# Optimization experiments

Measured on AMD Instinct MI355X. Metric: run time of the kernel, lower is better.

## Reference

```python
import jax, jax.numpy as jnp
import numpy as np


def _mha(q, k, v, num_heads):
    # q,k,v: [B, L, C] -> multi-head attention, scale = 1/sqrt(head_dim)
    B, Lq, C = q.shape
    Lk = k.shape[1]
    d = C // num_heads
    qh = q.reshape(B, Lq, num_heads, d)
    kh = k.reshape(B, Lk, num_heads, d)
    vh = v.reshape(B, Lk, num_heads, d)
    scale = 1.0 / jnp.sqrt(jnp.asarray(d, q.dtype))
    scores = jnp.einsum('blhd,bmhd->bhlm', qh, kh) * scale
    probs = jax.nn.softmax(scores, axis=-1)
    out = jnp.einsum('bhlm,bmhd->blhd', probs, vh)
    return out.reshape(B, Lq, C)


def setup_inputs() -> dict:
    key = jax.random.key(0)
    ks = jax.random.split(key, 9)
    b, n, f, l, C = 1, 4, 8, 256, 320
    s = 0.02
    return {
        'hidden_states': jax.random.normal(ks[0], (b * n * f, l, C), jnp.float32),
        'Wq': jax.random.normal(ks[1], (C, C), jnp.float32) * s,
        'Wk': jax.random.normal(ks[2], (C, C), jnp.float32) * s,
        'Wv': jax.random.normal(ks[3], (C, C), jnp.float32) * s,
        'Wo': jax.random.normal(ks[4], (C, C), jnp.float32) * s,
        'bo': jnp.zeros((C,), jnp.float32),
        'Wq_i2v': jax.random.normal(ks[5], (C, C), jnp.float32) * s,
        'Wo_i2v': jax.random.normal(ks[6], (C, C), jnp.float32) * s,
        'bo_i2v': jnp.zeros((C,), jnp.float32),
        'num_heads': 8,
        'num_views': 4,
        'num_frames': 8,
    }


def reference(hidden_states, Wq, Wk, Wv, Wo, bo, Wq_i2v, Wo_i2v, bo_i2v,
              num_heads, num_views, num_frames):
    BNF, l, C = hidden_states.shape
    n, f = num_views, num_frames
    b = BNF // (n * f)
    # '(b n f) l c -> (b f) (n l) c'
    h = hidden_states.reshape(b, n, f, l, C).transpose(0, 2, 1, 3, 4).reshape(b * f, n * l, C)
    L = n * l

    q = h @ Wq
    k = h @ Wk
    v = h @ Wv

    # first-frame KV broadcast across all frames within the same b
    k_first = jnp.broadcast_to(k.reshape(b, f, L, C)[:, 0:1], (b, f, L, C)).reshape(b * f, L, C)
    v_first = jnp.broadcast_to(v.reshape(b, f, L, C)[:, 0:1], (b, f, L, C)).reshape(b * f, L, C)

    base = _mha(q, k, v, num_heads)

    q_i2v = h @ Wq_i2v
    i2v = _mha(q_i2v, k_first, v_first, num_heads)
    i2v = i2v @ Wo_i2v + bo_i2v

    out = (base + i2v) @ Wo + bo

    # '(b f) (n l) c -> (b n f) l c'
    out = out.reshape(b, f, n, l, C).transpose(0, 2, 1, 3, 4).reshape(b * n * f, l, C)
    return out
```

## Files before the change

kernel.cpp:

```cpp
#include <hip/hip_runtime.h>
#include <hip/hip_bf16.h>

#define MROWS 8192
#define CDIM  320
#define QPAD  512

typedef __attribute__((ext_vector_type(8))) short bf16x8;
typedef __attribute__((ext_vector_type(4))) float f32x4;

__device__ __forceinline__ unsigned bfbits(float x) {
  union { float f; unsigned u; } a; a.f = x;
  return a.u + 0x8000u;
}
__device__ __forceinline__ void splitbf(float x, short& hi, short& lo) {
  unsigned hu = bfbits(x) & 0xffff0000u;
  union { unsigned u; float f; } h; h.u = hu;
  hi = (short)(hu >> 16);
  lo = (short)(bfbits(x - h.f) >> 16);
}
__device__ __forceinline__ unsigned pk_bf16(float a, float b) {
  union { __hip_bfloat162 h2; unsigned u; } cv;
  cv.h2 = __float22bfloat162_rn(float2{a, b});
  return cv.u;
}

__device__ __forceinline__ void cp16_g2l(const void* g, void* l) {
  __builtin_amdgcn_global_load_lds(
      (const __attribute__((address_space(1))) void*)g,
      (__attribute__((address_space(3))) void*)l, 16, 0, 0);
}

__device__ __forceinline__ int swizzle_row(int r) {
  int ff = r >> 10;
  int t  = r & 1023;
  int nn = t >> 8;
  int ll = t & 255;
  return nn * 2048 + ff * 256 + ll;
}

__global__ __launch_bounds__(256) void wc_kernel(
    const float* __restrict__ Woi, const float* __restrict__ Wo,
    float* __restrict__ Wc)
{
  const int r0 = blockIdx.x * 64, c0 = blockIdx.y * 64;
  __shared__ float As[64][36];
  __shared__ float Bs[32][68];
  const int tid = threadIdx.x, tx = tid & 15, ty = tid >> 4;
  float acc[4][4] = {};

  const int ra = tid >> 3, kq = (tid & 7) * 4;
  const int kb = tid >> 4, cq = (tid & 15) * 4;

  for (int k0 = 0; k0 < 320; k0 += 32) {
    float4 a1 = *(const float4*)(Woi + (size_t)(r0 + ra) * 320 + k0 + kq);
    float4 a2 = *(const float4*)(Woi + (size_t)(r0 + ra + 32) * 320 + k0 + kq);
    float4 b1 = *(const float4*)(Wo + (size_t)(k0 + kb) * 320 + c0 + cq);
    float4 b2 = *(const float4*)(Wo + (size_t)(k0 + kb + 16) * 320 + c0 + cq);
    __syncthreads();
    *(float4*)&As[ra][kq] = a1;
    *(float4*)&As[ra + 32][kq] = a2;
    *(float4*)&Bs[kb][cq] = b1;
    *(float4*)&Bs[kb + 16][cq] = b2;
    __syncthreads();
    #pragma unroll
    for (int kk = 0; kk < 32; ++kk) {
      float4 bv = *(const float4*)&Bs[kk][tx * 4];
      #pragma unroll
      for (int i = 0; i < 4; ++i) {
        float a = As[ty * 4 + i][kk];
        acc[i][0] = fmaf(a, bv.x, acc[i][0]);
        acc[i][1] = fmaf(a, bv.y, acc[i][1]);
        acc[i][2] = fmaf(a, bv.z, acc[i][2]);
        acc[i][3] = fmaf(a, bv.w, acc[i][3]);
      }
    }
  }
  #pragma unroll
  for (int i = 0; i < 4; ++i) {
    float4 v = make_float4(acc[i][0], acc[i][1], acc[i][2], acc[i][3]);
    *(float4*)(Wc + (size_t)(r0 + ty * 4 + i) * 320 + c0 + tx * 4) = v;
  }
}

__global__ __launch_bounds__(256) void pack_kernel(
    const float* __restrict__ hidden,
    const float* __restrict__ Wq, const float* __restrict__ Wk,
    const float* __restrict__ Wv, const float* __restrict__ Wqi,
    const float* __restrict__ Wo, const float* __restrict__ Wc,
    const float* __restrict__ bo, const float* __restrict__ boi,
    short* __restrict__ Ah, short* __restrict__ Al,
    short* __restrict__ WTh, short* __restrict__ WTl,
    short* __restrict__ WFh, short* __restrict__ WFl,
    float* __restrict__ bc,
    short* __restrict__ Qp, short* __restrict__ Kp, short* __restrict__ Qip,
    float qscale)
{
  const int b = blockIdx.x, tid = threadIdx.x;
  if (b < 64) {
    const int r0 = b * 128;
    for (int e = tid; e < 128 * 80; e += 256) {
      int r = e / 80, cq = (e % 80) * 4;
      float4 x = *(const float4*)(hidden + (size_t)swizzle_row(r0 + r) * 320 + cq);
      union { ushort4 v; short s[4]; } h, l;
      splitbf(x.x, h.s[0], l.s[0]); splitbf(x.y, h.s[1], l.s[1]);
      splitbf(x.z, h.s[2], l.s[2]); splitbf(x.w, h.s[3], l.s[3]);
      *(ushort4*)&Ah[(size_t)(r0 + r) * 320 + cq] = h.v;
      *(ushort4*)&Al[(size_t)(r0 + r) * 320 + cq] = l.v;
    }
  } else if (b < 128) {
    const int t2 = b - 64, wi = t2 >> 4, seg = t2 & 15;
    const float* W = wi == 0 ? Wq : wi == 1 ? Wk : wi == 2 ? Wv : Wqi;
    const float s = (wi == 0 || wi == 3) ? qscale : 1.0f;
    short* th = WTh + (size_t)wi * 320 * 320;
    short* tl = WTl + (size_t)wi * 320 * 320;
    for (int e = tid; e < 20 * 320; e += 256) {
      int n = seg * 20 + e / 320, k = e % 320;
      short hi, lo;
      splitbf(W[(size_t)k * 320 + n] * s, hi, lo);
      th[(size_t)n * 320 + k] = hi;
      tl[(size_t)n * 320 + k] = lo;
    }
  } else if (b < 160) {
    const int t2 = b - 128;
    for (int e = tid; e < 10 * 640; e += 256) {
      int n = t2 * 10 + e / 640, k = e % 640;
      float x = (k < 320) ? Wo[(size_t)k * 320 + n] : Wc[(size_t)(k - 320) * 320 + n];
      short hi, lo;
      splitbf(x, hi, lo);
      WFh[(size_t)n * 640 + k] = hi;
      WFl[(size_t)n * 640 + k] = lo;
    }
  } else if (b < 168) {
    const int n = (b - 160) * 40 + tid;
    if (tid < 40) {
      float s = bo[n];
      for (int j = 0; j < 320; ++j) s = fmaf(boi[j], Wo[(size_t)j * 320 + n], s);
      bc[n] = s;
    }
  } else {
    const int bz = b - 168, buf = bz >> 5, seg = bz & 31;
    short* P = buf == 0 ? Qp : buf == 1 ? Kp : Qip;
    const uint4 z = make_uint4(0, 0, 0, 0);
    for (int e = tid; e < 256 * 24; e += 256) {
      int row = (seg << 8) + (e / 24);
      int cc = e % 24, h = cc / 3, c3 = cc % 3;
      *(uint4*)&P[(size_t)row * QPAD + h * 64 + 40 + c3 * 8] = z;
    }
  }
}

__global__ __launch_bounds__(256, 3) void mfma_gemm(
    const short* __restrict__ Ah, const short* __restrict__ Al,
    const short* __restrict__ BTh, const short* __restrict__ BTl,
    int K, int mode,
    short* __restrict__ Qp, short* __restrict__ Kp,
    short* __restrict__ Vt, short* __restrict__ Qip,
    float* __restrict__ Of, const float* __restrict__ bias)
{
  const int tid  = threadIdx.x;
  const int wave = tid >> 6;
  const int lane = tid & 63;
  const int quad = lane >> 4;
  const int l16  = lane & 15;
  const int row0 = blockIdx.x * 128;

  const short *bth, *btl;
  int nbase, wi = 0;
  if (mode == 0) {
    const int ct = blockIdx.y;
    wi = ct / 5;
    bth = BTh + (size_t)wi * 320 * 320;
    btl = BTl + (size_t)wi * 320 * 320;
    nbase = (ct % 5) * 64;
  } else {
    bth = BTh; btl = BTl;
    nbase = blockIdx.y * 64;
  }

  __shared__ short Ash[128][32], Asl[128][32];
  __shared__ short Bsh[64][32],  Bsl[64][32];

  f32x4 acc[2][4];
  #pragma unroll
  for (int mt = 0; mt < 2; ++mt)
    #pragma unroll
    for (int nt = 0; nt < 4; ++nt) acc[mt][nt] = (f32x4){0.f, 0.f, 0.f, 0.f};

  const int lr = lane >> 2, lc = (lane & 3) * 8;
  const short* gah = Ah + (size_t)(row0 + wave * 16 + lr) * K + lc;
  const short* gal = Al ? Al + (size_t)(row0 + wave * 16 + lr) * K + lc : nullptr;
  const short* gbh = bth + (size_t)(nbase + wave * 16 + lr) * K + lc;
  const short* gbl = btl + (size_t)(nbase + wave * 16 + lr) * K + lc;
  short* lah1 = &Ash[wave * 16][0];
  short* lah2 = &Ash[64 + wave * 16][0];
  short* lal1 = &Asl[wave * 16][0];
  short* lal2 = &Asl[64 + wave * 16][0];
  short* lbh  = &Bsh[wave * 16][0];
  short* lbl  = &Bsl[wave * 16][0];

  for (int k0 = 0; k0 < K; k0 += 32) {
    __syncthreads();
    cp16_g2l(gah + k0, lah1);
    cp16_g2l(gah + (size_t)64 * K + k0, lah2);
    if (Al) {
      cp16_g2l(gal + k0, lal1);
      cp16_g2l(gal + (size_t)64 * K + k0, lal2);
    }
    cp16_g2l(gbh + k0, lbh);
    cp16_g2l(gbl + k0, lbl);
    __syncthreads();

    bf16x8 afh[2], afl[2], bfh[4], bfl[4];
    #pragma unroll
    for (int mt = 0; mt < 2; ++mt) {
      afh[mt] = *(const bf16x8*)&Ash[wave * 32 + mt * 16 + l16][quad * 8];
      if (Al) afl[mt] = *(const bf16x8*)&Asl[wave * 32 + mt * 16 + l16][quad * 8];
    }
    #pragma unroll
    for (int nt = 0; nt < 4; ++nt) {
      bfh[nt] = *(const bf16x8*)&Bsh[nt * 16 + l16][quad * 8];
      bfl[nt] = *(const bf16x8*)&Bsl[nt * 16 + l16][quad * 8];
    }
    #pragma unroll
    for (int mt = 0; mt < 2; ++mt)
      #pragma unroll
      for (int nt = 0; nt < 4; ++nt) {
        acc[mt][nt] = __builtin_amdgcn_mfma_f32_16x16x32_bf16(afh[mt], bfh[nt], acc[mt][nt], 0, 0, 0);
        acc[mt][nt] = __builtin_amdgcn_mfma_f32_16x16x32_bf16(afh[mt], bfl[nt], acc[mt][nt], 0, 0, 0);
        if (Al)
          acc[mt][nt] = __builtin_amdgcn_mfma_f32_16x16x32_bf16(afl[mt], bfh[nt], acc[mt][nt], 0, 0, 0);
      }
  }

  if (mode == 0) {
    if (wi == 2) {
      #pragma unroll
      for (int mt = 0; mt < 2; ++mt)
        #pragma unroll
        for (int nt = 0; nt < 4; ++nt) {
          const int col  = nbase + nt * 16 + l16;
          const int rowb = row0 + wave * 32 + mt * 16 + quad * 4;
          union { ushort4 v; short s[4]; } pk;
          #pragma unroll
          for (int r = 0; r < 4; ++r) pk.s[r] = (short)(bfbits(acc[mt][nt][r]) >> 16);
          *(ushort4*)&Vt[(size_t)col * MROWS + rowb] = pk.v;
        }
    } else {
      short* Op = wi == 0 ? Qp : wi == 1 ? Kp : Qip;
      #pragma unroll
      for (int mt = 0; mt < 2; ++mt)
        #pragma unroll
        for (int nt = 0; nt < 4; ++nt) {
          const int col  = nbase + nt * 16 + l16;
          const int h    = col / 40;
          const int pcol = h * 64 + (col - h * 40);
          const int rowb = row0 + wave * 32 + mt * 16 + quad * 4;
          #pragma unroll
          for (int r = 0; r < 4; ++r)
            Op[(size_t)(rowb + r) * QPAD + pcol] = (short)(bfbits(acc[mt][nt][r]) >> 16);
        }
    }
  } else {
    #pragma unroll
    for (int mt = 0; mt < 2; ++mt)
      #pragma unroll
      for (int nt = 0; nt < 4; ++nt) {
        const int col  = nbase + nt * 16 + l16;
        const int rowb = row0 + wave * 32 + mt * 16 + quad * 4;
        const float bb = bias[col];
        #pragma unroll
        for (int r = 0; r < 4; ++r)
          Of[(size_t)swizzle_row(rowb + r) * CDIM + col] = acc[mt][nt][r] + bb;
      }
  }
}

__global__ __launch_bounds__(256, 4) void attn_kernel(
    const short* __restrict__ Qp, const short* __restrict__ Qip,
    const short* __restrict__ Kp, const short* __restrict__ Vtg,
    short* __restrict__ AOh)
{
  const int lid  = blockIdx.x;
  const int qblk = lid >> 7;
  const int t7   = lid & 127;
  const int hh   = t7 & 7;
  const int zz   = t7 >> 3;
  const int var  = zz >> 3;
  const int bf   = zz & 7;
  const int tid  = threadIdx.x;
  const int wave = tid >> 6;
  const int lane = tid & 63;
  const int quad = lane >> 4;
  const int l16  = lane & 15;

  const short* Q = var ? Qip : Qp;
  const int kvbase = var ? 0 : (bf << 10);
  const int coff = var * 320 + hh * 40;

  __shared__ short Ks[2][64][64];
  __shared__ short Vt[2][48][64];
  __shared__ short Ps[4][16][68];

  if (tid < 128) {
    const int bsel = tid >> 6, t6 = tid & 63;
    const int pr = t6 >> 3;
    uint4 fill = (pr == 0) ? make_uint4(0x3F803F80u, 0x3F803F80u, 0x3F803F80u, 0x3F803F80u)
                           : make_uint4(0, 0, 0, 0);
    *(uint4*)&Vt[bsel][40 + pr][(t6 & 7) * 8] = fill;
  }

  bf16x8 qf0[2], qf1[2];
  #pragma unroll
  for (int qt = 0; qt < 2; ++qt) {
    const short* qp = Q + (size_t)((bf << 10) + (qblk << 7) + (wave << 5) + (qt << 4) + l16) * QPAD + hh * 64;
    qf0[qt] = *(const bf16x8*)(qp + quad * 8);
    qf1[qt] = *(const bf16x8*)(qp + 32 + quad * 8);
  }

  f32x4 acc[2][3];
  #pragma unroll
  for (int qt = 0; qt < 2; ++qt)
    #pragma unroll
    for (int t = 0; t < 3; ++t) acc[qt][t] = (f32x4){0.f, 0.f, 0.f, 0.f};

  const short* Kb = Kp + (size_t)kvbase * QPAD + hh * 64;
  const short* Vb = Vtg + (size_t)(hh * 40) * MROWS + kvbase;

  const int lrow = lane >> 3;
  const int gch  = ((lane & 7) ^ (lrow & 7)) * 8;
  const int sw   = l16 & 7;

  auto stage = [&](int s0, int bsel) {
    #pragma unroll
    for (int j = 0; j < 4; ++j) {
      const int u = j * 4 + wave;
      if (u < 8) {
        cp16_g2l(Kb + (size_t)(s0 + u * 8 + lrow) * QPAD + gch, &Ks[bsel][u * 8][0]);
      } else if (u < 13) {
        cp16_g2l(Vb + (size_t)((u - 8) * 8 + lrow) * MROWS + s0 + gch, &Vt[bsel][(u - 8) * 8][0]);
      }
    }
  };

  auto compute = [&](int bsel) {
    bf16x8 vf[2][3];
    #pragma unroll
    for (int kh = 0; kh < 2; ++kh)
      #pragma unroll
      for (int t = 0; t < 3; ++t)
        vf[kh][t] = *(const bf16x8*)&Vt[bsel][t * 16 + l16][((kh * 4 + quad) ^ sw) * 8];

    #pragma unroll
    for (int qt = 0; qt < 2; ++qt) {
      #pragma unroll
      for (int kt = 0; kt < 4; ++kt) {
        const short* kr = &Ks[bsel][kt * 16 + l16][0];
        bf16x8 kb0 = *(const bf16x8*)(kr + (quad ^ sw) * 8);
        bf16x8 kb1 = *(const bf16x8*)(kr + ((quad + 4) ^ sw) * 8);
        f32x4 st = (f32x4){0.f, 0.f, 0.f, 0.f};
        __builtin_amdgcn_s_setprio(1);
        st = __builtin_amdgcn_mfma_f32_16x16x32_bf16(kb0, qf0[qt], st, 0, 0, 0);
        st = __builtin_amdgcn_mfma_f32_16x16x32_bf16(kb1, qf1[qt], st, 0, 0, 0);
        __builtin_amdgcn_s_setprio(0);
        float p0 = __builtin_amdgcn_exp2f(st[0]);
        float p1 = __builtin_amdgcn_exp2f(st[1]);
        float p2 = __builtin_amdgcn_exp2f(st[2]);
        float p3 = __builtin_amdgcn_exp2f(st[3]);
        uint2 pk;
        pk.x = pk_bf16(p0, p1);
        pk.y = pk_bf16(p2, p3);
        *(uint2*)&Ps[wave][l16][kt * 16 + quad * 4] = pk;
      }

      asm volatile("s_waitcnt lgkmcnt(0)" ::: "memory");

      bf16x8 pa0 = *(const bf16x8*)&Ps[wave][l16][quad * 8];
      bf16x8 pa1 = *(const bf16x8*)&Ps[wave][l16][32 + quad * 8];
      __builtin_amdgcn_s_setprio(1);
      #pragma unroll
      for (int t = 0; t < 3; ++t) {
        acc[qt][t] = __builtin_amdgcn_mfma_f32_16x16x32_bf16(pa0, vf[0][t], acc[qt][t], 0, 0, 0);
        acc[qt][t] = __builtin_amdgcn_mfma_f32_16x16x32_bf16(pa1, vf[1][t], acc[qt][t], 0, 0, 0);
      }
      __builtin_amdgcn_s_setprio(0);
    }
  };

  stage(0, 0);
  __syncthreads();

  #pragma unroll 1
  for (int s0 = 0; s0 < 1024; s0 += 128) {
    stage(s0 + 64, 1);
    compute(0);
    __syncthreads();
    if (s0 + 128 < 1024) stage(s0 + 128, 0);
    compute(1);
    __syncthreads();
  }

  #pragma unroll
  for (int qt = 0; qt < 2; ++qt) {
    float invr[4];
    #pragma unroll
    for (int r = 0; r < 4; ++r) {
      float d = __shfl(acc[qt][2][r], quad * 16 + 8, 64);
      invr[r] = 1.f / d;
    }

    const int baserow = (bf << 10) + (qblk << 7) + (wave << 5) + (qt << 4) + quad * 4;
    #pragma unroll
    for (int t = 0; t < 3; ++t) {
      int dcol = t * 16 + l16;
      if (dcol < 40) {
        short* op = AOh + (size_t)baserow * 640 + coff + dcol;
        #pragma unroll
        for (int r = 0; r < 4; ++r)
          op[(size_t)r * 640] = (short)(bfbits(acc[qt][t][r] * invr[r]) >> 16);
      }
    }
  }
}

extern "C" void kernel_launch(void* const* d_in, const int* in_sizes, int n_in,
                              void* d_out, int out_size, void* d_ws, size_t ws_size,
                              hipStream_t stream) {
  const float* hidden  = (const float*)d_in[0];
  const float* Wq      = (const float*)d_in[1];
  const float* Wk      = (const float*)d_in[2];
  const float* Wv      = (const float*)d_in[3];
  const float* Wo      = (const float*)d_in[4];
  const float* bo      = (const float*)d_in[5];
  const float* Wq_i2v  = (const float*)d_in[6];
  const float* Wo_i2v  = (const float*)d_in[7];
  const float* bo_i2v  = (const float*)d_in[8];
  float* out = (float*)d_out;

  const size_t SZ  = (size_t)MROWS * CDIM;
  const size_t SZP = (size_t)MROWS * QPAD;
  short* Ah  = (short*)d_ws;
  short* Al  = Ah + SZ;
  short* AOh = Ah;
  short* Qp  = Al + SZ;
  short* Kp  = Qp + SZP;
  short* Qip = Kp + SZP;
  short* Vt  = Qip + SZP;
  short* WTh = Vt + (size_t)328 * MROWS;
  short* WTl = WTh + 409600;
  short* WFh = WTl + 409600;
  short* WFl = WFh + 204800;
  float* Wc  = (float*)(WFl + 204800);
  float* bc  = Wc + 102400;

  const float qscale = 0.22811011717177393f;

  wc_kernel<<<dim3(5, 5), 256, 0, stream>>>(Wo_i2v, Wo, Wc);

  pack_kernel<<<dim3(264), 256, 0, stream>>>(
      hidden, Wq, Wk, Wv, Wq_i2v, Wo, Wc, bo, bo_i2v,
      Ah, Al, WTh, WTl, WFh, WFl, bc, Qp, Kp, Qip, qscale);

  mfma_gemm<<<dim3(64, 20), 256, 0, stream>>>(
      Ah, Al, WTh, WTl, 320, 0, Qp, Kp, Vt, Qip, nullptr, nullptr);

  attn_kernel<<<dim3(1024), 256, 0, stream>>>(Qp, Qip, Kp, Vt, AOh);

  mfma_gemm<<<dim3(64, 5), 256, 0, stream>>>(
      AOh, nullptr, WFh, WFl, 640, 1, nullptr, nullptr, nullptr, nullptr, out, bc);
}
```

Before: 202.0 us.

## Switch attention kernel to 32x32x16 MFMA with register-resident P via permlane32 swap

Rewrites the attention inner loop to use 32x32x16 bf16 MFMA tiles instead of 16x16x32. The softmax probabilities now stay in registers, reshuffled with permlane32_swap instead of a round trip through shared memory. The aim is to cut LDS traffic and the number of MFMA issues, at the cost of padding the head dimension to 64 in V, which wastes some compute. Register pressure rises, so launch bounds drop to 3 blocks per SM.

```diff
diff --git a/kernel.cpp b/kernel.cpp
--- a/kernel.cpp
+++ b/kernel.cpp
@@ -7,6 +7,7 @@
 
 typedef __attribute__((ext_vector_type(8))) short bf16x8;
 typedef __attribute__((ext_vector_type(4))) float f32x4;
+typedef __attribute__((ext_vector_type(16))) float f32x16;
 
 __device__ __forceinline__ unsigned bfbits(float x) {
   union { float f; unsigned u; } a; a.f = x;
@@ -275,60 +276,58 @@
   }
 }
 
-__global__ __launch_bounds__(256, 4) void attn_kernel(
+__global__ __launch_bounds__(256, 3) void attn_kernel(
     const short* __restrict__ Qp, const short* __restrict__ Qip,
     const short* __restrict__ Kp, const short* __restrict__ Vtg,
     short* __restrict__ AOh)
 {
   const int lid  = blockIdx.x;
+  const int hh   = lid & 7;
+  const int zz   = (lid >> 3) & 15;
   const int qblk = lid >> 7;
-  const int t7   = lid & 127;
-  const int hh   = t7 & 7;
-  const int zz   = t7 >> 3;
   const int var  = zz >> 3;
   const int bf   = zz & 7;
   const int tid  = threadIdx.x;
   const int wave = tid >> 6;
   const int lane = tid & 63;
-  const int quad = lane >> 4;
-  const int l16  = lane & 15;
+  const int hi   = lane >> 5;
+  const int l31  = lane & 31;
 
   const short* Q = var ? Qip : Qp;
   const int kvbase = var ? 0 : (bf << 10);
   const int coff = var * 320 + hh * 40;
 
   __shared__ short Ks[2][64][64];
-  __shared__ short Vt[2][48][64];
-  __shared__ short Ps[4][16][68];
-
-  if (tid < 128) {
-    const int bsel = tid >> 6, t6 = tid & 63;
-    const int pr = t6 >> 3;
-    uint4 fill = (pr == 0) ? make_uint4(0x3F803F80u, 0x3F803F80u, 0x3F803F80u, 0x3F803F80u)
-                           : make_uint4(0, 0, 0, 0);
-    *(uint4*)&Vt[bsel][40 + pr][(t6 & 7) * 8] = fill;
-  }
-
-  bf16x8 qf0[2], qf1[2];
+  __shared__ short Vs[2][64][64];
+
+  for (int e = tid; e < 384; e += 256) {
+    const int bsel = e >= 192, t = e - bsel * 192;
+    const int row = 40 + (t >> 3), ch = t & 7;
+    uint4 fill = (row == 40) ? make_uint4(0x3F803F80u, 0x3F803F80u, 0x3F803F80u, 0x3F803F80u)
+                             : make_uint4(0, 0, 0, 0);
+    *(uint4*)&Vs[bsel][row][ch * 8] = fill;
+  }
+
+  const int qbase = (bf << 10) + (qblk << 7) + (wave << 5);
+  bf16x8 qf[3];
+  {
+    const short* qp = Q + (size_t)(qbase + l31) * QPAD + hh * 64 + hi * 8;
+    qf[0] = *(const bf16x8*)(qp);
+    qf[1] = *(const bf16x8*)(qp + 16);
+    qf[2] = *(const bf16x8*)(qp + 32);
+  }
+
+  f32x16 acc[2];
   #pragma unroll
-  for (int qt = 0; qt < 2; ++qt) {
-    const short* qp = Q + (size_t)((bf << 10) + (qblk << 7) + (wave << 5) + (qt << 4) + l16) * QPAD + hh * 64;
-    qf0[qt] = *(const bf16x8*)(qp + quad * 8);
-    qf1[qt] = *(const bf16x8*)(qp + 32 + quad * 8);
-  }
-
-  f32x4 acc[2][3];
-  #pragma unroll
-  for (int qt = 0; qt < 2; ++qt)
-    #pragma unroll
-    for (int t = 0; t < 3; ++t) acc[qt][t] = (f32x4){0.f, 0.f, 0.f, 0.f};
+  for (int dt = 0; dt < 2; ++dt)
+    #pragma unroll
+    for (int r = 0; r < 16; ++r) acc[dt][r] = 0.f;
 
   const short* Kb = Kp + (size_t)kvbase * QPAD + hh * 64;
   const short* Vb = Vtg + (size_t)(hh * 40) * MROWS + kvbase;
 
   const int lrow = lane >> 3;
   const int gch  = ((lane & 7) ^ (lrow & 7)) * 8;
-  const int sw   = l16 & 7;
 
   auto stage = [&](int s0, int bsel) {
     #pragma unroll
@@ -337,53 +336,80 @@
       if (u < 8) {
         cp16_g2l(Kb + (size_t)(s0 + u * 8 + lrow) * QPAD + gch, &Ks[bsel][u * 8][0]);
       } else if (u < 13) {
-        cp16_g2l(Vb + (size_t)((u - 8) * 8 + lrow) * MROWS + s0 + gch, &Vt[bsel][(u - 8) * 8][0]);
+        cp16_g2l(Vb + (size_t)((u - 8) * 8 + lrow) * MROWS + s0 + gch, &Vs[bsel][(u - 8) * 8][0]);
       }
     }
   };
 
+  auto plswap = [&](unsigned& a, unsigned& b) {
+#if __has_builtin(__builtin_amdgcn_permlane32_swap)
+    auto r = __builtin_amdgcn_permlane32_swap(a, b, false, false);
+    unsigned na = (unsigned)r[0], nb = (unsigned)r[1];
+    a = na; b = nb;
+#else
+    unsigned as = (unsigned)__shfl((int)a, lane ^ 32, 64);
+    unsigned bs = (unsigned)__shfl((int)b, lane ^ 32, 64);
+    unsigned na = hi ? bs : a;
+    unsigned nb = hi ? b : as;
+    a = na; b = nb;
+#endif
+  };
+
   auto compute = [&](int bsel) {
-    bf16x8 vf[2][3];
-    #pragma unroll
-    for (int kh = 0; kh < 2; ++kh)
-      #pragma unroll
-      for (int t = 0; t < 3; ++t)
-        vf[kh][t] = *(const bf16x8*)&Vt[bsel][t * 16 + l16][((kh * 4 + quad) ^ sw) * 8];
-
-    #pragma unroll
-    for (int qt = 0; qt < 2; ++qt) {
-      #pragma unroll
-      for (int kt = 0; kt < 4; ++kt) {
-        const short* kr = &Ks[bsel][kt * 16 + l16][0];
-        bf16x8 kb0 = *(const bf16x8*)(kr + (quad ^ sw) * 8);
-        bf16x8 kb1 = *(const bf16x8*)(kr + ((quad + 4) ^ sw) * 8);
-        f32x4 st = (f32x4){0.f, 0.f, 0.f, 0.f};
-        __builtin_amdgcn_s_setprio(1);
-        st = __builtin_amdgcn_mfma_f32_16x16x32_bf16(kb0, qf0[qt], st, 0, 0, 0);
-        st = __builtin_amdgcn_mfma_f32_16x16x32_bf16(kb1, qf1[qt], st, 0, 0, 0);
-        __builtin_amdgcn_s_setprio(0);
-        float p0 = __builtin_amdgcn_exp2f(st[0]);
-        float p1 = __builtin_amdgcn_exp2f(st[1]);
-        float p2 = __builtin_amdgcn_exp2f(st[2]);
-        float p3 = __builtin_amdgcn_exp2f(st[3]);
-        uint2 pk;
-        pk.x = pk_bf16(p0, p1);
-        pk.y = pk_bf16(p2, p3);
-        *(uint2*)&Ps[wave][l16][kt * 16 + quad * 4] = pk;
-      }
-
-      asm volatile("s_waitcnt lgkmcnt(0)" ::: "memory");
-
-      bf16x8 pa0 = *(const bf16x8*)&Ps[wave][l16][quad * 8];
-      bf16x8 pa1 = *(const bf16x8*)&Ps[wave][l16][32 + quad * 8];
+    bf16x8 vf[2][4];
+    #pragma unroll
+    for (int dt = 0; dt < 2; ++dt) {
+      const int vrow = dt * 32 + l31;
+      #pragma unroll
+      for (int kc = 0; kc < 4; ++kc)
+        vf[dt][kc] = *(const bf16x8*)&Vs[bsel][vrow][((((kc << 1) | hi) ^ (vrow & 7)) << 3)];
+    }
+
+    bf16x8 pa[4];
+    #pragma unroll
+    for (int kt2 = 0; kt2 < 2; ++kt2) {
+      const int krow = kt2 * 32 + l31;
+      bf16x8 kf0 = *(const bf16x8*)&Ks[bsel][krow][((((0 << 1) | hi) ^ (krow & 7)) << 3)];
+      bf16x8 kf1 = *(const bf16x8*)&Ks[bsel][krow][((((1 << 1) | hi) ^ (krow & 7)) << 3)];
+      bf16x8 kf2 = *(const bf16x8*)&Ks[bsel][krow][((((2 << 1) | hi) ^ (krow & 7)) << 3)];
+
+      f32x16 S;
+      #pragma unroll
+      for (int r = 0; r < 16; ++r) S[r] = 0.f;
       __builtin_amdgcn_s_setprio(1);
-      #pragma unroll
-      for (int t = 0; t < 3; ++t) {
-        acc[qt][t] = __builtin_amdgcn_mfma_f32_16x16x32_bf16(pa0, vf[0][t], acc[qt][t], 0, 0, 0);
-        acc[qt][t] = __builtin_amdgcn_mfma_f32_16x16x32_bf16(pa1, vf[1][t], acc[qt][t], 0, 0, 0);
-      }
+      S = __builtin_amdgcn_mfma_f32_32x32x16_bf16(kf0, qf[0], S, 0, 0, 0);
+      S = __builtin_amdgcn_mfma_f32_32x32x16_bf16(kf1, qf[1], S, 0, 0, 0);
+      S = __builtin_amdgcn_mfma_f32_32x32x16_bf16(kf2, qf[2], S, 0, 0, 0);
       __builtin_amdgcn_s_setprio(0);
-    }
+
+      float p[16];
+      #pragma unroll
+      for (int r = 0; r < 16; ++r) p[r] = __builtin_amdgcn_exp2f(S[r]);
+
+      unsigned w01 = pk_bf16(p[0], p[1]),  w23 = pk_bf16(p[2], p[3]);
+      unsigned w45 = pk_bf16(p[4], p[5]),  w67 = pk_bf16(p[6], p[7]);
+      plswap(w01, w45);
+      plswap(w23, w67);
+      union { unsigned u[4]; bf16x8 v; } t0;
+      t0.u[0] = w01; t0.u[1] = w23; t0.u[2] = w45; t0.u[3] = w67;
+      pa[kt2 * 2] = t0.v;
+
+      unsigned x01 = pk_bf16(p[8], p[9]),   x23 = pk_bf16(p[10], p[11]);
+      unsigned x45 = pk_bf16(p[12], p[13]), x67 = pk_bf16(p[14], p[15]);
+      plswap(x01, x45);
+      plswap(x23, x67);
+      union { unsigned u[4]; bf16x8 v; } t1;
+      t1.u[0] = x01; t1.u[1] = x23; t1.u[2] = x45; t1.u[3] = x67;
+      pa[kt2 * 2 + 1] = t1.v;
+    }
+
+    __builtin_amdgcn_s_setprio(1);
+    #pragma unroll
+    for (int kc = 0; kc < 4; ++kc) {
+      acc[0] = __builtin_amdgcn_mfma_f32_32x32x16_bf16(pa[kc], vf[0][kc], acc[0], 0, 0, 0);
+      acc[1] = __builtin_amdgcn_mfma_f32_32x32x16_bf16(pa[kc], vf[1][kc], acc[1], 0, 0, 0);
+    }
+    __builtin_amdgcn_s_setprio(0);
   };
 
   stage(0, 0);
@@ -399,24 +425,22 @@
     __syncthreads();
   }
 
+  float inv[16];
   #pragma unroll
-  for (int qt = 0; qt < 2; ++qt) {
-    float invr[4];
-    #pragma unroll
-    for (int r = 0; r < 4; ++r) {
-      float d = __shfl(acc[qt][2][r], quad * 16 + 8, 64);
-      invr[r] = 1.f / d;
-    }
-
-    const int baserow = (bf << 10) + (qblk << 7) + (wave << 5) + (qt << 4) + quad * 4;
-    #pragma unroll
-    for (int t = 0; t < 3; ++t) {
-      int dcol = t * 16 + l16;
-      if (dcol < 40) {
-        short* op = AOh + (size_t)baserow * 640 + coff + dcol;
-        #pragma unroll
-        for (int r = 0; r < 4; ++r)
-          op[(size_t)r * 640] = (short)(bfbits(acc[qt][t][r] * invr[r]) >> 16);
+  for (int r = 0; r < 16; ++r) {
+    float d = __shfl(acc[1][r], (lane & 32) | 8, 64);
+    inv[r] = 1.f / d;
+  }
+
+  #pragma unroll
+  for (int dt = 0; dt < 2; ++dt) {
+    const int d = dt * 32 + l31;
+    if (d < 40) {
+      short* op = AOh + (size_t)qbase * 640 + coff + d;
+      #pragma unroll
+      for (int r = 0; r < 16; ++r) {
+        const int qoff = (r & 3) + 8 * (r >> 2) + 4 * hi;
+        op[(size_t)qoff * 640] = (short)(bfbits(acc[dt][r] * inv[r]) >> 16);
       }
     }
   }
```

After: 203.2 us. Within noise of the previous version (+0.6%).
